# Performance work log

Hardware: AMD Instinct MI355X
Metric: run time of the kernel (lower is better)

The kernel has to match this reference:

```python
import jax, jax.numpy as jnp
import numpy as np

N_NODES = 50000
N_EDGES = 800000
D_IN = 128
D_HID = 128
D_OUT = 1
N_GRAPHS = 64


def gcn_conv(x, edge_index, W, b):
    """PyG GCNConv: add self-loops, symmetric deg^-1/2 normalization, xW, scatter-add, +bias."""
    n = x.shape[0]
    loops = jnp.arange(n, dtype=edge_index.dtype)
    row = jnp.concatenate([edge_index[0], loops])  # source nodes
    col = jnp.concatenate([edge_index[1], loops])  # destination nodes
    deg = jax.ops.segment_sum(jnp.ones_like(col, dtype=x.dtype), col, num_segments=n)
    dinv = jax.lax.rsqrt(jnp.maximum(deg, 1.0))  # deg >= 1 due to self-loops
    norm = dinv[row] * dinv[col]                 # [E+N]
    h = x @ W                                    # [N, d_out] dense GEMM first (cheaper than per-edge)
    msgs = h[row] * norm[:, None]                # gather + scale, [E+N, d_out]
    out = jax.ops.segment_sum(msgs, col, num_segments=n)  # scatter-add
    return out + b


def setup_inputs() -> dict:
    key = jax.random.key(0)
    ks = jax.random.split(key, 12)
    x = jax.random.normal(ks[0], (N_NODES, D_IN), dtype=jnp.float32)
    edge_index = jax.random.randint(ks[1], (2, N_EDGES), 0, N_NODES, dtype=jnp.int64)
    batch = jnp.sort(jax.random.randint(ks[2], (N_NODES,), 0, N_GRAPHS, dtype=jnp.int64))
    s_in = 1.0 / np.sqrt(D_IN)
    s_hid = 1.0 / np.sqrt(D_HID)
    W0 = jax.random.uniform(ks[3], (D_IN, D_HID), jnp.float32, -s_in, s_in)
    b0 = jnp.zeros((D_HID,), jnp.float32)
    W1 = jax.random.uniform(ks[4], (D_HID, D_HID), jnp.float32, -s_hid, s_hid)
    b1 = jnp.zeros((D_HID,), jnp.float32)
    W2 = jax.random.uniform(ks[5], (D_HID, D_HID), jnp.float32, -s_hid, s_hid)
    b2 = jnp.zeros((D_HID,), jnp.float32)
    fc_w = jax.random.uniform(ks[6], (D_HID, D_OUT), jnp.float32, -s_hid, s_hid)
    fc_b = jax.random.uniform(ks[7], (D_OUT,), jnp.float32, -s_hid, s_hid)
    return {"x": x, "edge_index": edge_index, "batch": batch,
            "W0": W0, "b0": b0, "W1": W1, "b1": b1, "W2": W2, "b2": b2,
            "fc_w": fc_w, "fc_b": fc_b}


def reference(x, edge_index, batch, W0, b0, W1, b1, W2, b2, fc_w, fc_b):
    h = x
    for W, b in ((W0, b0), (W1, b1), (W2, b2)):  # 3 GCN layers (structural, not data loop)
        h = jax.nn.relu(gcn_conv(h, edge_index, W, b))
    # global_mean_pool over graph ids
    sums = jax.ops.segment_sum(h, batch, num_segments=N_GRAPHS)          # [G, d]
    counts = jax.ops.segment_sum(jnp.ones((h.shape[0],), h.dtype), batch, num_segments=N_GRAPHS)
    pooled = sums / jnp.maximum(counts, 1.0)[:, None]
    return pooled @ fc_w + fc_b  # [G, 1]
```

## Files before the change

kernel.cpp:

```cpp
#include <hip/hip_runtime.h>

#define DH 128
#define NGRAPH 64
#define SLOT_CAP 64

static __device__ __forceinline__ float4 f4fma(float a, float4 b, float4 c) {
  c.x = fmaf(a, b.x, c.x); c.y = fmaf(a, b.y, c.y);
  c.z = fmaf(a, b.z, c.z); c.w = fmaf(a, b.w, c.w);
  return c;
}

template<bool SCALE>
static __device__ __forceinline__ void gemm_body(const float* __restrict__ A, const float* __restrict__ W,
                                                 const float* __restrict__ dinv, float* __restrict__ C,
                                                 int M, int blk) {
  __shared__ float ws4[32][128];
  const int tid = threadIdx.x;
  const int tx = tid & 31;
  const int ty = tid >> 5;
  const int m_base = blk * 64;

  const float* ar[8];
  #pragma unroll
  for (int i = 0; i < 8; i++) {
    int r = m_base + ty * 8 + i;
    if (r >= M) r = M - 1;
    ar[i] = A + (size_t)r * DH;
  }

  float4 acc[8];
  #pragma unroll
  for (int i = 0; i < 8; i++) acc[i] = make_float4(0.f, 0.f, 0.f, 0.f);

  for (int kc = 0; kc < 128; kc += 32) {
    const float4* Wg = (const float4*)(W + kc * DH);
    float4* wsv = (float4*)ws4;
    wsv[tid] = Wg[tid];
    wsv[tid + 256] = Wg[tid + 256];
    wsv[tid + 512] = Wg[tid + 512];
    wsv[tid + 768] = Wg[tid + 768];
    __syncthreads();
    #pragma unroll
    for (int k = 0; k < 32; k += 4) {
      float4 wb0 = *(const float4*)&ws4[k + 0][tx * 4];
      float4 wb1 = *(const float4*)&ws4[k + 1][tx * 4];
      float4 wb2 = *(const float4*)&ws4[k + 2][tx * 4];
      float4 wb3 = *(const float4*)&ws4[k + 3][tx * 4];
      #pragma unroll
      for (int i = 0; i < 8; i++) {
        float4 xa = *(const float4*)(ar[i] + kc + k);
        acc[i] = f4fma(xa.x, wb0, acc[i]);
        acc[i] = f4fma(xa.y, wb1, acc[i]);
        acc[i] = f4fma(xa.z, wb2, acc[i]);
        acc[i] = f4fma(xa.w, wb3, acc[i]);
      }
    }
    __syncthreads();
  }
  #pragma unroll
  for (int i = 0; i < 8; i++) {
    int r = m_base + ty * 8 + i;
    if (SCALE) {
      int rc = (r < M) ? r : (M - 1);
      float dsc = dinv[rc];
      acc[i].x *= dsc; acc[i].y *= dsc; acc[i].z *= dsc; acc[i].w *= dsc;
    }
    *(float4*)(C + (size_t)r * DH + tx * 4) = acc[i];
  }
}

__global__ __launch_bounds__(256) void megaA_k(const float* __restrict__ x, const float* __restrict__ W0,
                                               float* __restrict__ bufA, int M,
                                               const int* __restrict__ row, const int* __restrict__ col,
                                               int* __restrict__ cnt, int* __restrict__ csr_src,
                                               const int* __restrict__ batch, int* __restrict__ gcnt,
                                               int e, int n, int nblocks) {
  int vb = blockIdx.x;
  if (vb % 5 == 0) {
    gemm_body<false>(x, W0, nullptr, bufA, M, vb / 5);
    return;
  }
  int bi = vb - vb / 5 - 1;
  int i = bi * 256 + threadIdx.x;
  if (i < e) {
    int c = col[i];
    int pos = atomicAdd(&cnt[c], 1);
    if (pos < SLOT_CAP) csr_src[(size_t)c * SLOT_CAP + pos] = row[i];
  }
  bool active = (i < n);
  int g = active ? batch[i] : 0;
  unsigned long long act = __ballot(active);
  if (!active) return;
  int first = __ffsll((long long)act) - 1;
  int g0 = __shfl(g, first);
  bool uni = __all(g == g0);
  int lane = threadIdx.x & 63;
  if (uni) {
    if (lane == first) atomicAdd(&gcnt[g], (int)__popcll(act));
  } else {
    atomicAdd(&gcnt[g], 1);
  }
}

__global__ __launch_bounds__(256) void post_k(const int* __restrict__ cnt, float* __restrict__ dinv,
                                              float* __restrict__ bufA, int n) {
  int r = blockIdx.x * 8 + (threadIdx.x >> 5);
  int lane = threadIdx.x & 31;
  if (r >= n) return;
  float d = rsqrtf((float)(cnt[r] + 1));
  if (lane == 0) dinv[r] = d;
  float4* p = (float4*)bufA + (size_t)r * 32 + lane;
  float4 v = *p;
  v.x *= d; v.y *= d; v.z *= d; v.w *= d;
  *p = v;
}

__global__ __launch_bounds__(256) void gemm_scaled_k(const float* __restrict__ A, const float* __restrict__ W,
                                                     const float* __restrict__ dinv,
                                                     float* __restrict__ C, int M) {
  gemm_body<true>(A, W, dinv, C, M, blockIdx.x);
}

__global__ __launch_bounds__(256) void aggregate_k(const float* __restrict__ hs, const float* __restrict__ dinv,
                                                   const int* __restrict__ cnt, const int* __restrict__ csr_src,
                                                   const float* __restrict__ bias, float* __restrict__ out, int n) {
  int wave = threadIdx.x >> 6;
  int lane = threadIdx.x & 63;
  int node = blockIdx.x * 4 + wave;
  if (node >= n) return;
  const float2* h2 = (const float2*)hs;
  float di = dinv[node];
  int m = cnt[node]; if (m > SLOT_CAP) m = SLOT_CAP;
  const int* lst = csr_src + (size_t)node * SLOT_CAP;
  float2 a0 = h2[(size_t)node * 64 + lane];
  float2 a1 = make_float2(0.f, 0.f), a2 = a1, a3 = a1, a4 = a1, a5 = a1, a6 = a1, a7 = a1;
  int e = 0;
  for (; e + 8 <= m; e += 8) {
    int s0 = lst[e + 0], s1 = lst[e + 1], s2 = lst[e + 2], s3 = lst[e + 3];
    int s4 = lst[e + 4], s5 = lst[e + 5], s6 = lst[e + 6], s7 = lst[e + 7];
    float2 v0 = h2[(size_t)s0 * 64 + lane];
    float2 v1 = h2[(size_t)s1 * 64 + lane];
    float2 v2 = h2[(size_t)s2 * 64 + lane];
    float2 v3 = h2[(size_t)s3 * 64 + lane];
    float2 v4 = h2[(size_t)s4 * 64 + lane];
    float2 v5 = h2[(size_t)s5 * 64 + lane];
    float2 v6 = h2[(size_t)s6 * 64 + lane];
    float2 v7 = h2[(size_t)s7 * 64 + lane];
    a0.x += v0.x; a0.y += v0.y;
    a1.x += v1.x; a1.y += v1.y;
    a2.x += v2.x; a2.y += v2.y;
    a3.x += v3.x; a3.y += v3.y;
    a4.x += v4.x; a4.y += v4.y;
    a5.x += v5.x; a5.y += v5.y;
    a6.x += v6.x; a6.y += v6.y;
    a7.x += v7.x; a7.y += v7.y;
  }
  for (; e + 4 <= m; e += 4) {
    int s0 = lst[e + 0], s1 = lst[e + 1], s2 = lst[e + 2], s3 = lst[e + 3];
    float2 v0 = h2[(size_t)s0 * 64 + lane];
    float2 v1 = h2[(size_t)s1 * 64 + lane];
    float2 v2 = h2[(size_t)s2 * 64 + lane];
    float2 v3 = h2[(size_t)s3 * 64 + lane];
    a0.x += v0.x; a0.y += v0.y;
    a1.x += v1.x; a1.y += v1.y;
    a2.x += v2.x; a2.y += v2.y;
    a3.x += v3.x; a3.y += v3.y;
  }
  for (; e < m; ++e) {
    int s = lst[e];
    float2 v = h2[(size_t)s * 64 + lane];
    a0.x += v.x; a0.y += v.y;
  }
  float sx = ((a0.x + a1.x) + (a2.x + a3.x)) + ((a4.x + a5.x) + (a6.x + a7.x));
  float sy = ((a0.y + a1.y) + (a2.y + a3.y)) + ((a4.y + a5.y) + (a6.y + a7.y));
  float2 b = *(const float2*)(bias + lane * 2);
  sx = fmaxf(fmaf(sx, di, b.x), 0.f);
  sy = fmaxf(fmaf(sy, di, b.y), 0.f);
  ((float2*)out)[(size_t)node * 64 + lane] = make_float2(sx, sy);
}

#define POOL_CHUNK 50
__global__ __launch_bounds__(128) void pool_partial_k(const float* __restrict__ h, const int* __restrict__ batch,
                                                      float* __restrict__ pooled, int n) {
  int n0 = blockIdx.x * POOL_CHUNK;
  if (n0 >= n) return;
  int n1 = n0 + POOL_CHUNK; if (n1 > n) n1 = n;
  int d = threadIdx.x;
  float acc = 0.f;
  int gp = batch[n0];
  for (int i = n0; i < n1; ++i) {
    int g = batch[i];
    if (g != gp) { atomicAdd(&pooled[(size_t)gp * DH + d], acc); acc = 0.f; gp = g; }
    acc += h[(size_t)i * DH + d];
  }
  atomicAdd(&pooled[(size_t)gp * DH + d], acc);
}

__global__ void final_k(const float* __restrict__ pooled, const int* __restrict__ gcnt,
                        const float* __restrict__ fcw, const float* __restrict__ fcb,
                        float* __restrict__ out) {
  int g = threadIdx.x;
  if (g >= NGRAPH) return;
  float c = fmaxf((float)gcnt[g], 1.f);
  float s = 0.f;
  #pragma unroll 4
  for (int d = 0; d < DH; ++d) s = fmaf(pooled[(size_t)g * DH + d] / c, fcw[d], s);
  out[g] = s + fcb[0];
}

extern "C" void kernel_launch(void* const* d_in, const int* in_sizes, int n_in,
                              void* d_out, int out_size, void* d_ws, size_t ws_size,
                              hipStream_t stream) {
  const float* x    = (const float*)d_in[0];
  const int*   ei   = (const int*)d_in[1];
  const int*   batch= (const int*)d_in[2];
  const float* W0   = (const float*)d_in[3];
  const float* b0   = (const float*)d_in[4];
  const float* W1   = (const float*)d_in[5];
  const float* b1   = (const float*)d_in[6];
  const float* W2   = (const float*)d_in[7];
  const float* b2   = (const float*)d_in[8];
  const float* fcw  = (const float*)d_in[9];
  const float* fcb  = (const float*)d_in[10];
  float* out = (float*)d_out;

  const int N = in_sizes[0] / DH;
  const int E = in_sizes[1] / 2;
  const int* row = ei;
  const int* col = ei + E;
  const int MPAD = ((N + 63) / 64) * 64;

  char* ws = (char*)d_ws;
  size_t off = 0;
  auto carve = [&](size_t bytes) -> char* {
    char* p = ws + off;
    off = (off + bytes + 255) & ~(size_t)255;
    return p;
  };
  float* bufA    = (float*)carve((size_t)MPAD * DH * 4);
  float* bufB    = (float*)carve((size_t)MPAD * DH * 4);
  int*   cnt     = (int*)carve((size_t)N * 4);
  float* dinv    = (float*)carve((size_t)N * 4);
  int*   csr_src = (int*)carve((size_t)N * SLOT_CAP * 4);
  int*   gcnt    = (int*)carve(NGRAPH * 4);
  float* pooled  = (float*)carve((size_t)NGRAPH * DH * 4);
  (void)ws_size; (void)n_in; (void)out_size;

  const int CB = (E + 255) / 256;
  const int gemmBlocks = MPAD / 64;
  const int NB = gemmBlocks + CB;
  const int aggBlocks = (N + 3) / 4;

  hipMemsetAsync(cnt, 0, (size_t)N * 4, stream);
  hipMemsetAsync(gcnt, 0, NGRAPH * 4 + (size_t)NGRAPH * DH * 4, stream);

  megaA_k<<<NB, 256, 0, stream>>>(x, W0, bufA, N, row, col, cnt, csr_src, batch, gcnt, E, N, NB);
  post_k<<<(N + 7) / 8, 256, 0, stream>>>(cnt, dinv, bufA, N);

  aggregate_k<<<aggBlocks, 256, 0, stream>>>(bufA, dinv, cnt, csr_src, b0, bufB, N);
  gemm_scaled_k<<<gemmBlocks, 256, 0, stream>>>(bufB, W1, dinv, bufA, N);
  aggregate_k<<<aggBlocks, 256, 0, stream>>>(bufA, dinv, cnt, csr_src, b1, bufB, N);
  gemm_scaled_k<<<gemmBlocks, 256, 0, stream>>>(bufB, W2, dinv, bufA, N);
  aggregate_k<<<aggBlocks, 256, 0, stream>>>(bufA, dinv, cnt, csr_src, b2, bufB, N);

  const int poolBlocks = (N + POOL_CHUNK - 1) / POOL_CHUNK;
  pool_partial_k<<<poolBlocks, 128, 0, stream>>>(bufB, batch, pooled, N);
  final_k<<<1, 64, 0, stream>>>(pooled, gcnt, fcw, fcb, out);
}
```

Baseline: 473.0 us.

## Split fused GEMM/scatter kernel and use float4 half-wave gathers in aggregation

The interleaved first GEMM plus edge-scatter megakernel is split into two separate launches. The aggregation kernel now has each half-wave gather a different neighbour row with float4 loads, doing two edges per wave step, and combines the halves with a cross-half shuffle. The wider loads and two rows in flight per step are meant to raise memory-level parallelism in the gather-bound aggregation. In exchange there is one more launch, the GEMM and scatter no longer overlap, and the final write uses only half the lanes.

```diff
diff --git a/kernel.cpp b/kernel.cpp
--- a/kernel.cpp
+++ b/kernel.cpp
@@ -69,19 +69,22 @@
   }
 }
 
-__global__ __launch_bounds__(256) void megaA_k(const float* __restrict__ x, const float* __restrict__ W0,
-                                               float* __restrict__ bufA, int M,
-                                               const int* __restrict__ row, const int* __restrict__ col,
-                                               int* __restrict__ cnt, int* __restrict__ csr_src,
-                                               const int* __restrict__ batch, int* __restrict__ gcnt,
-                                               int e, int n, int nblocks) {
-  int vb = blockIdx.x;
-  if (vb % 5 == 0) {
-    gemm_body<false>(x, W0, nullptr, bufA, M, vb / 5);
-    return;
-  }
-  int bi = vb - vb / 5 - 1;
-  int i = bi * 256 + threadIdx.x;
+__global__ __launch_bounds__(256) void gemm1_k(const float* __restrict__ x, const float* __restrict__ W0,
+                                               float* __restrict__ bufA, int M) {
+  gemm_body<false>(x, W0, nullptr, bufA, M, blockIdx.x);
+}
+
+__global__ __launch_bounds__(256) void gemm_scaled_k(const float* __restrict__ A, const float* __restrict__ W,
+                                                     const float* __restrict__ dinv,
+                                                     float* __restrict__ C, int M) {
+  gemm_body<true>(A, W, dinv, C, M, blockIdx.x);
+}
+
+__global__ void scatter_k(const int* __restrict__ row, const int* __restrict__ col,
+                          int* __restrict__ cnt, int* __restrict__ csr_src,
+                          const int* __restrict__ batch, int* __restrict__ gcnt,
+                          int e, int n) {
+  int i = blockIdx.x * blockDim.x + threadIdx.x;
   if (i < e) {
     int c = col[i];
     int pos = atomicAdd(&cnt[c], 1);
@@ -115,68 +118,64 @@
   *p = v;
 }
 
-__global__ __launch_bounds__(256) void gemm_scaled_k(const float* __restrict__ A, const float* __restrict__ W,
-                                                     const float* __restrict__ dinv,
-                                                     float* __restrict__ C, int M) {
-  gemm_body<true>(A, W, dinv, C, M, blockIdx.x);
-}
-
 __global__ __launch_bounds__(256) void aggregate_k(const float* __restrict__ hs, const float* __restrict__ dinv,
                                                    const int* __restrict__ cnt, const int* __restrict__ csr_src,
                                                    const float* __restrict__ bias, float* __restrict__ out, int n) {
   int wave = threadIdx.x >> 6;
   int lane = threadIdx.x & 63;
+  int half = lane >> 5;
+  int l32 = lane & 31;
   int node = blockIdx.x * 4 + wave;
   if (node >= n) return;
-  const float2* h2 = (const float2*)hs;
+  const float4* h4 = (const float4*)hs;
   float di = dinv[node];
   int m = cnt[node]; if (m > SLOT_CAP) m = SLOT_CAP;
   const int* lst = csr_src + (size_t)node * SLOT_CAP;
-  float2 a0 = h2[(size_t)node * 64 + lane];
-  float2 a1 = make_float2(0.f, 0.f), a2 = a1, a3 = a1, a4 = a1, a5 = a1, a6 = a1, a7 = a1;
+  float4 a0 = make_float4(0.f, 0.f, 0.f, 0.f), a1 = a0, a2 = a0, a3 = a0;
   int e = 0;
   for (; e + 8 <= m; e += 8) {
-    int s0 = lst[e + 0], s1 = lst[e + 1], s2 = lst[e + 2], s3 = lst[e + 3];
-    int s4 = lst[e + 4], s5 = lst[e + 5], s6 = lst[e + 6], s7 = lst[e + 7];
-    float2 v0 = h2[(size_t)s0 * 64 + lane];
-    float2 v1 = h2[(size_t)s1 * 64 + lane];
-    float2 v2 = h2[(size_t)s2 * 64 + lane];
-    float2 v3 = h2[(size_t)s3 * 64 + lane];
-    float2 v4 = h2[(size_t)s4 * 64 + lane];
-    float2 v5 = h2[(size_t)s5 * 64 + lane];
-    float2 v6 = h2[(size_t)s6 * 64 + lane];
-    float2 v7 = h2[(size_t)s7 * 64 + lane];
-    a0.x += v0.x; a0.y += v0.y;
-    a1.x += v1.x; a1.y += v1.y;
-    a2.x += v2.x; a2.y += v2.y;
-    a3.x += v3.x; a3.y += v3.y;
-    a4.x += v4.x; a4.y += v4.y;
-    a5.x += v5.x; a5.y += v5.y;
-    a6.x += v6.x; a6.y += v6.y;
-    a7.x += v7.x; a7.y += v7.y;
-  }
-  for (; e + 4 <= m; e += 4) {
-    int s0 = lst[e + 0], s1 = lst[e + 1], s2 = lst[e + 2], s3 = lst[e + 3];
-    float2 v0 = h2[(size_t)s0 * 64 + lane];
-    float2 v1 = h2[(size_t)s1 * 64 + lane];
-    float2 v2 = h2[(size_t)s2 * 64 + lane];
-    float2 v3 = h2[(size_t)s3 * 64 + lane];
-    a0.x += v0.x; a0.y += v0.y;
-    a1.x += v1.x; a1.y += v1.y;
-    a2.x += v2.x; a2.y += v2.y;
-    a3.x += v3.x; a3.y += v3.y;
-  }
-  for (; e < m; ++e) {
+    int s0 = lst[e + 0 + half];
+    int s1 = lst[e + 2 + half];
+    int s2 = lst[e + 4 + half];
+    int s3 = lst[e + 6 + half];
+    float4 v0 = h4[(size_t)s0 * 32 + l32];
+    float4 v1 = h4[(size_t)s1 * 32 + l32];
+    float4 v2 = h4[(size_t)s2 * 32 + l32];
+    float4 v3 = h4[(size_t)s3 * 32 + l32];
+    a0.x += v0.x; a0.y += v0.y; a0.z += v0.z; a0.w += v0.w;
+    a1.x += v1.x; a1.y += v1.y; a1.z += v1.z; a1.w += v1.w;
+    a2.x += v2.x; a2.y += v2.y; a2.z += v2.z; a2.w += v2.w;
+    a3.x += v3.x; a3.y += v3.y; a3.z += v3.z; a3.w += v3.w;
+  }
+  for (; e + 2 <= m; e += 2) {
+    int s = lst[e + half];
+    float4 v = h4[(size_t)s * 32 + l32];
+    a0.x += v.x; a0.y += v.y; a0.z += v.z; a0.w += v.w;
+  }
+  if (e < m && half == 0) {
     int s = lst[e];
-    float2 v = h2[(size_t)s * 64 + lane];
-    a0.x += v.x; a0.y += v.y;
-  }
-  float sx = ((a0.x + a1.x) + (a2.x + a3.x)) + ((a4.x + a5.x) + (a6.x + a7.x));
-  float sy = ((a0.y + a1.y) + (a2.y + a3.y)) + ((a4.y + a5.y) + (a6.y + a7.y));
-  float2 b = *(const float2*)(bias + lane * 2);
-  sx = fmaxf(fmaf(sx, di, b.x), 0.f);
-  sy = fmaxf(fmaf(sy, di, b.y), 0.f);
-  ((float2*)out)[(size_t)node * 64 + lane] = make_float2(sx, sy);
+    float4 v = h4[(size_t)s * 32 + l32];
+    a0.x += v.x; a0.y += v.y; a0.z += v.z; a0.w += v.w;
+  }
+  float4 s4;
+  s4.x = (a0.x + a1.x) + (a2.x + a3.x);
+  s4.y = (a0.y + a1.y) + (a2.y + a3.y);
+  s4.z = (a0.z + a1.z) + (a2.z + a3.z);
+  s4.w = (a0.w + a1.w) + (a2.w + a3.w);
+  s4.x += __shfl_xor(s4.x, 32);
+  s4.y += __shfl_xor(s4.y, 32);
+  s4.z += __shfl_xor(s4.z, 32);
+  s4.w += __shfl_xor(s4.w, 32);
+  if (half == 0) {
+    float4 self = h4[(size_t)node * 32 + l32];
+    float4 b = ((const float4*)bias)[l32];
+    float4 r;
+    r.x = fmaxf(fmaf(s4.x + self.x, di, b.x), 0.f);
+    r.y = fmaxf(fmaf(s4.y + self.y, di, b.y), 0.f);
+    r.z = fmaxf(fmaf(s4.z + self.z, di, b.z), 0.f);
+    r.w = fmaxf(fmaf(s4.w + self.w, di, b.w), 0.f);
+    ((float4*)out)[(size_t)node * 32 + l32] = r;
+  }
 }
 
 #define POOL_CHUNK 50
@@ -248,13 +247,13 @@
 
   const int CB = (E + 255) / 256;
   const int gemmBlocks = MPAD / 64;
-  const int NB = gemmBlocks + CB;
   const int aggBlocks = (N + 3) / 4;
 
   hipMemsetAsync(cnt, 0, (size_t)N * 4, stream);
   hipMemsetAsync(gcnt, 0, NGRAPH * 4 + (size_t)NGRAPH * DH * 4, stream);
 
-  megaA_k<<<NB, 256, 0, stream>>>(x, W0, bufA, N, row, col, cnt, csr_src, batch, gcnt, E, N, NB);
+  gemm1_k<<<gemmBlocks, 256, 0, stream>>>(x, W0, bufA, N);
+  scatter_k<<<CB, 256, 0, stream>>>(row, col, cnt, csr_src, batch, gcnt, E, N);
   post_k<<<(N + 7) / 8, 256, 0, stream>>>(cnt, dinv, bufA, N);
 
   aggregate_k<<<aggBlocks, 256, 0, stream>>>(bufA, dinv, cnt, csr_src, b0, bufB, N);
```

Result: no change. 477.8 us (+1.0%).
